# Kernel optimization log

Measured on AMD Instinct MI355X. Metric: run time of the kernel, lower is better.

## Reference

```python
import jax, jax.numpy as jnp
import numpy as np
from functools import partial

NUM_STEPS = 30  # Euler integration steps (inte_steps)


def _point_sample(vol, pts):
    """Trilinear sample of vol [C,D,H,W] at pts [N,3] (voxel coords, (d,h,w) order).
    Matches torch grid_sample(mode='bilinear', padding_mode='border', align_corners=True)
    after the normalize+flip done in PointPooling. Returns [C,N]."""
    dims = jnp.asarray(vol.shape[1:], dtype=pts.dtype)  # (D,H,W)
    p = jnp.clip(pts, 0.0, dims - 1.0)  # border padding == clamp coords
    p0 = jnp.floor(p)
    frac = p - p0  # [N,3]
    i0 = p0.astype(jnp.int32)
    i1 = jnp.minimum(i0 + 1, (dims - 1.0).astype(jnp.int32))
    d0, h0, w0 = i0[:, 0], i0[:, 1], i0[:, 2]
    d1, h1, w1 = i1[:, 0], i1[:, 1], i1[:, 2]
    fd, fh, fw = frac[:, 0], frac[:, 1], frac[:, 2]
    g = lambda d, h, w: vol[:, d, h, w]  # [C,N] gather
    c000, c001 = g(d0, h0, w0), g(d0, h0, w1)
    c010, c011 = g(d0, h1, w0), g(d0, h1, w1)
    c100, c101 = g(d1, h0, w0), g(d1, h0, w1)
    c110, c111 = g(d1, h1, w0), g(d1, h1, w1)
    c00 = c000 * (1 - fw) + c001 * fw
    c01 = c010 * (1 - fw) + c011 * fw
    c10 = c100 * (1 - fw) + c101 * fw
    c11 = c110 * (1 - fw) + c111 * fw
    c0 = c00 * (1 - fh) + c01 * fh
    c1 = c10 * (1 - fh) + c11 * fh
    return c0 * (1 - fd) + c1 * fd  # [C,N]


def _interp(flow, x):
    # flow [B,3,D,H,W], x [B,N,3] -> [B,N,3]
    out = jax.vmap(_point_sample)(flow, x)  # [B,3,N]
    return jnp.transpose(out, (0, 2, 1))


def _integrate_euler(flow, x, num_steps):
    flow = flow * (1.0 / num_steps)
    def step(x, _):
        return x + _interp(flow, x), None
    x, _ = jax.lax.scan(step, x, None, length=num_steps)
    return x


def _forward(verts, affine, flow_field):
    B, N, _ = verts.shape
    ones = jnp.ones((B, N, 1), dtype=verts.dtype)
    homog = jnp.concatenate([verts, ones], axis=-1)  # [B,N,4]
    pred = jnp.einsum('bij,bnj->bni', affine, homog)[..., :3]
    aux = _integrate_euler(flow_field, pred, NUM_STEPS)
    flow_int = aux - pred  # [B,N,3]
    pred = aux
    flow_int = jnp.transpose(flow_int, (0, 2, 1))[..., None, None]  # [B,3,N,1,1]
    homog2 = jnp.concatenate([pred, ones], axis=-1)
    inv_aff = jnp.linalg.inv(affine)
    pred = jnp.einsum('bij,bnj->bni', inv_aff, homog2)[..., :3]
    return pred, flow_int


def setup_inputs() -> dict:
    key = jax.random.key(0)
    k1, k2, k3 = jax.random.split(key, 3)
    B, N = 2, 140000
    D = H = W = 192
    dims = jnp.asarray([D - 1, H - 1, W - 1], dtype=jnp.float32)
    verts = jax.random.uniform(k1, (B, N, 3), dtype=jnp.float32) * dims
    affine = jnp.eye(4, dtype=jnp.float32)[None] + 0.01 * jax.random.normal(k2, (B, 4, 4), dtype=jnp.float32)
    flow_field = jax.random.normal(k3, (B, 3, D, H, W), dtype=jnp.float32)
    return {"verts": verts, "affine": affine, "flow_field": flow_field}


def reference(verts, affine, flow_field):
    return _forward(verts, affine, flow_field)
```

## Files before the change

### kernel.cpp

```cpp
#include <hip/hip_runtime.h>
#include <hip/hip_fp16.h>

#define NSTEPS 30
#define DIM 192
static constexpr long DHW = (long)DIM * DIM * DIM;
static constexpr int PTS_PER_WAVE = 21;

__global__ void invert4x4_kernel(const float* __restrict__ aff,
                                 float* __restrict__ out, int B) {
    int b = blockIdx.x * blockDim.x + threadIdx.x;
    if (b >= B) return;
    double a[16];
#pragma unroll
    for (int i = 0; i < 16; i++) a[i] = (double)aff[b * 16 + i];
    double s0 = a[0]*a[5]  - a[4]*a[1];
    double s1 = a[0]*a[6]  - a[4]*a[2];
    double s2 = a[0]*a[7]  - a[4]*a[3];
    double s3 = a[1]*a[6]  - a[5]*a[2];
    double s4 = a[1]*a[7]  - a[5]*a[3];
    double s5 = a[2]*a[7]  - a[6]*a[3];
    double c5 = a[10]*a[15] - a[14]*a[11];
    double c4 = a[9]*a[15]  - a[13]*a[11];
    double c3 = a[9]*a[14]  - a[13]*a[10];
    double c2 = a[8]*a[15]  - a[12]*a[11];
    double c1 = a[8]*a[14]  - a[12]*a[10];
    double c0 = a[8]*a[13]  - a[12]*a[9];
    double det = s0*c5 - s1*c4 + s2*c3 + s3*c2 - s4*c1 + s5*c0;
    double inv = 1.0 / det;
    double o[16];
    o[0]  = ( a[5]*c5 - a[6]*c4 + a[7]*c3) * inv;
    o[1]  = (-a[1]*c5 + a[2]*c4 - a[3]*c3) * inv;
    o[2]  = ( a[13]*s5 - a[14]*s4 + a[15]*s3) * inv;
    o[3]  = (-a[9]*s5 + a[10]*s4 - a[11]*s3) * inv;
    o[4]  = (-a[4]*c5 + a[6]*c2 - a[7]*c1) * inv;
    o[5]  = ( a[0]*c5 - a[2]*c2 + a[3]*c1) * inv;
    o[6]  = (-a[12]*s5 + a[14]*s2 - a[15]*s1) * inv;
    o[7]  = ( a[8]*s5 - a[10]*s2 + a[11]*s1) * inv;
    o[8]  = ( a[4]*c4 - a[5]*c2 + a[7]*c0) * inv;
    o[9]  = (-a[0]*c4 + a[1]*c2 - a[3]*c0) * inv;
    o[10] = ( a[12]*s4 - a[13]*s2 + a[15]*s0) * inv;
    o[11] = (-a[8]*s4 + a[9]*s2 - a[11]*s0) * inv;
    o[12] = (-a[4]*c3 + a[5]*c1 - a[6]*c0) * inv;
    o[13] = ( a[0]*c3 - a[1]*c1 + a[2]*c0) * inv;
    o[14] = (-a[12]*s3 + a[13]*s1 - a[14]*s0) * inv;
    o[15] = ( a[8]*s3 - a[9]*s1 + a[10]*s0) * inv;
#pragma unroll
    for (int i = 0; i < 16; i++) out[b * 16 + i] = (float)o[i];
}

__global__ __launch_bounds__(256) void repack_kernel(const float* __restrict__ flow,
                                                     __half* __restrict__ packed) {
    long vox = (long)blockIdx.x * blockDim.x + threadIdx.x;
    int b = blockIdx.y;
    if (vox >= DHW) return;
    const float* F = flow + (size_t)b * 3 * DHW;
    float f0 = F[vox];
    float f1 = F[vox + DHW];
    float f2 = F[vox + 2 * DHW];
    union { __half2 h2[2]; int2 i2; } u;
    u.h2[0] = __floats2half2_rn(f0, f1);
    u.h2[1] = __floats2half2_rn(f2, 0.0f);
    reinterpret_cast<int2*>(packed)[(size_t)b * DHW + vox] = u.i2;
}

__global__ __launch_bounds__(256) void deform_packed_kernel(
    const float* __restrict__ verts,
    const float* __restrict__ affine,
    const __half* __restrict__ packed,
    const float* __restrict__ invaff,
    float* __restrict__ out_pred,
    float* __restrict__ out_flow,
    int N, int B) {
    int lane = threadIdx.x & 63;
    int wib  = threadIdx.x >> 6;
    long gwave = (long)blockIdx.x * (blockDim.x >> 6) + wib;

    int piw = lane / 3;
    if (piw > PTS_PER_WAVE - 1) piw = PTS_PER_WAVE - 1;
    int ch = lane - piw * 3;
    if (ch > 2) ch = 2;

    long pt = gwave * PTS_PER_WAVE + piw;
    bool valid = (lane < 63) && (pt < (long)B * N);
    long ptc = valid ? pt : ((long)B * N - 1);
    int b = (int)(ptc / N);
    int n = (int)(ptc - (long)b * N);

    const float* A = affine + b * 16;
    const float* v = verts + (size_t)ptc * 3;
    float vx = v[0], vy = v[1], vz = v[2];
    float x = A[0] * vx + A[1] * vy + A[2]  * vz + A[3];
    float y = A[4] * vx + A[5] * vy + A[6]  * vz + A[7];
    float z = A[8] * vx + A[9] * vy + A[10] * vz + A[11];
    float p0 = (ch == 0) ? x : (ch == 1) ? y : z;

    const __half* Pb = packed + ((size_t)b * DHW) * 4 + ch;
    const float scale = (float)(1.0 / NSTEPS);

    float cc[8];
    int key = -1;
    int bl = piw * 3;

    for (int s = 0; s < NSTEPS; s++) {
        float pd = fminf(fmaxf(x, 0.0f), (float)(DIM - 1));
        float ph = fminf(fmaxf(y, 0.0f), (float)(DIM - 1));
        float pw = fminf(fmaxf(z, 0.0f), (float)(DIM - 1));
        float fd0 = floorf(pd), fh0 = floorf(ph), fw0 = floorf(pw);
        int d0 = (int)fd0, h0 = (int)fh0, w0 = (int)fw0;
        float fd = pd - fd0, fh = ph - fh0, fw = pw - fw0;

        int k = (d0 * DIM + h0) * DIM + w0;
        if (k != key) {
            key = k;
            int d1 = min(d0 + 1, DIM - 1);
            int h1 = min(h0 + 1, DIM - 1);
            int w1 = min(w0 + 1, DIM - 1);
            size_t r00 = (size_t)((d0 * DIM + h0) * DIM) * 4;
            size_t r01 = (size_t)((d0 * DIM + h1) * DIM) * 4;
            size_t r10 = (size_t)((d1 * DIM + h0) * DIM) * 4;
            size_t r11 = (size_t)((d1 * DIM + h1) * DIM) * 4;
            size_t o0 = (size_t)w0 * 4, o1 = (size_t)w1 * 4;
            cc[0] = __half2float(Pb[r00 + o0]) * scale;
            cc[1] = __half2float(Pb[r00 + o1]) * scale;
            cc[2] = __half2float(Pb[r01 + o0]) * scale;
            cc[3] = __half2float(Pb[r01 + o1]) * scale;
            cc[4] = __half2float(Pb[r10 + o0]) * scale;
            cc[5] = __half2float(Pb[r10 + o1]) * scale;
            cc[6] = __half2float(Pb[r11 + o0]) * scale;
            cc[7] = __half2float(Pb[r11 + o1]) * scale;
        }

        float omfw = 1.0f - fw, omfh = 1.0f - fh, omfd = 1.0f - fd;
        float c00 = cc[0] * omfw + cc[1] * fw;
        float c01 = cc[2] * omfw + cc[3] * fw;
        float c10 = cc[4] * omfw + cc[5] * fw;
        float c11 = cc[6] * omfw + cc[7] * fw;
        float c0 = c00 * omfh + c01 * fh;
        float c1 = c10 * omfh + c11 * fh;
        float val = c0 * omfd + c1 * fd;

        float v0 = __shfl(val, bl,     64);
        float v1 = __shfl(val, bl + 1, 64);
        float v2 = __shfl(val, bl + 2, 64);
        x += v0; y += v1; z += v2;
    }

    if (valid) {
        float posc = (ch == 0) ? x : (ch == 1) ? y : z;
        float fint = posc - p0;
        const float* Ai = invaff + b * 16 + ch * 4;
        float o = Ai[0] * x + Ai[1] * y + Ai[2] * z + Ai[3];
        out_pred[(size_t)ptc * 3 + ch] = o;
        out_flow[(size_t)b * 3 * N + (size_t)ch * N + n] = fint;
    }
}

__global__ __launch_bounds__(256) void deform_kernel(
    const float* __restrict__ verts,
    const float* __restrict__ affine,
    const float* __restrict__ flow,
    const float* __restrict__ invaff,
    float* __restrict__ out_pred,
    float* __restrict__ out_flow,
    int N, int B) {
    int lane = threadIdx.x & 63;
    int wib  = threadIdx.x >> 6;
    long gwave = (long)blockIdx.x * (blockDim.x >> 6) + wib;
    int piw = lane / 3;
    if (piw > PTS_PER_WAVE - 1) piw = PTS_PER_WAVE - 1;
    int ch = lane - piw * 3;
    if (ch > 2) ch = 2;
    long pt = gwave * PTS_PER_WAVE + piw;
    bool valid = (lane < 63) && (pt < (long)B * N);
    long ptc = valid ? pt : ((long)B * N - 1);
    int b = (int)(ptc / N);
    int n = (int)(ptc - (long)b * N);
    const float* A = affine + b * 16;
    const float* v = verts + (size_t)ptc * 3;
    float vx = v[0], vy = v[1], vz = v[2];
    float x = A[0] * vx + A[1] * vy + A[2]  * vz + A[3];
    float y = A[4] * vx + A[5] * vy + A[6]  * vz + A[7];
    float z = A[8] * vx + A[9] * vy + A[10] * vz + A[11];
    float p0 = (ch == 0) ? x : (ch == 1) ? y : z;
    const float* Fc = flow + ((size_t)b * 3 + ch) * (size_t)DHW;
    const float scale = (float)(1.0 / NSTEPS);
    float cc[8];
    int key = -1;
    int bl = piw * 3;
    for (int s = 0; s < NSTEPS; s++) {
        float pd = fminf(fmaxf(x, 0.0f), (float)(DIM - 1));
        float ph = fminf(fmaxf(y, 0.0f), (float)(DIM - 1));
        float pw = fminf(fmaxf(z, 0.0f), (float)(DIM - 1));
        float fd0 = floorf(pd), fh0 = floorf(ph), fw0 = floorf(pw);
        int d0 = (int)fd0, h0 = (int)fh0, w0 = (int)fw0;
        float fd = pd - fd0, fh = ph - fh0, fw = pw - fw0;
        int k = (d0 * DIM + h0) * DIM + w0;
        if (k != key) {
            key = k;
            int d1 = min(d0 + 1, DIM - 1);
            int h1 = min(h0 + 1, DIM - 1);
            int w1 = min(w0 + 1, DIM - 1);
            int r00 = (d0 * DIM + h0) * DIM;
            int r01 = (d0 * DIM + h1) * DIM;
            int r10 = (d1 * DIM + h0) * DIM;
            int r11 = (d1 * DIM + h1) * DIM;
            cc[0] = Fc[r00 + w0] * scale;
            cc[1] = Fc[r00 + w1] * scale;
            cc[2] = Fc[r01 + w0] * scale;
            cc[3] = Fc[r01 + w1] * scale;
            cc[4] = Fc[r10 + w0] * scale;
            cc[5] = Fc[r10 + w1] * scale;
            cc[6] = Fc[r11 + w0] * scale;
            cc[7] = Fc[r11 + w1] * scale;
        }
        float omfw = 1.0f - fw, omfh = 1.0f - fh, omfd = 1.0f - fd;
        float c00 = cc[0] * omfw + cc[1] * fw;
        float c01 = cc[2] * omfw + cc[3] * fw;
        float c10 = cc[4] * omfw + cc[5] * fw;
        float c11 = cc[6] * omfw + cc[7] * fw;
        float c0 = c00 * omfh + c01 * fh;
        float c1 = c10 * omfh + c11 * fh;
        float val = c0 * omfd + c1 * fd;
        float v0 = __shfl(val, bl,     64);
        float v1 = __shfl(val, bl + 1, 64);
        float v2 = __shfl(val, bl + 2, 64);
        x += v0; y += v1; z += v2;
    }
    if (valid) {
        float posc = (ch == 0) ? x : (ch == 1) ? y : z;
        float fint = posc - p0;
        const float* Ai = invaff + b * 16 + ch * 4;
        float o = Ai[0] * x + Ai[1] * y + Ai[2] * z + Ai[3];
        out_pred[(size_t)ptc * 3 + ch] = o;
        out_flow[(size_t)b * 3 * N + (size_t)ch * N + n] = fint;
    }
}

extern "C" void kernel_launch(void* const* d_in, const int* in_sizes, int n_in,
                              void* d_out, int out_size, void* d_ws, size_t ws_size,
                              hipStream_t stream) {
    const float* verts  = (const float*)d_in[0];
    const float* affine = (const float*)d_in[1];
    const float* flow   = (const float*)d_in[2];

    int B = in_sizes[1] / 16;
    int N = in_sizes[0] / (3 * B);

    float* out_pred = (float*)d_out;
    float* out_flow = out_pred + (size_t)B * N * 3;

    size_t packed_bytes = (size_t)B * DHW * 4 * sizeof(__half);
    bool use_packed = (ws_size >= packed_bytes + 256);

    long total_pts = (long)B * N;
    long waves  = (total_pts + PTS_PER_WAVE - 1) / PTS_PER_WAVE;
    long blocks = (waves + 3) / 4;

    if (use_packed) {
        __half* packed = (__half*)d_ws;
        float* invaff  = (float*)((char*)d_ws + packed_bytes);
        hipLaunchKernelGGL(invert4x4_kernel, dim3(1), dim3(64), 0, stream,
                           affine, invaff, B);
        long vblocks = (DHW + 255) / 256;
        hipLaunchKernelGGL(repack_kernel, dim3((unsigned)vblocks, B), dim3(256), 0,
                           stream, flow, packed);
        hipLaunchKernelGGL(deform_packed_kernel, dim3((unsigned)blocks), dim3(256),
                           0, stream, verts, affine, packed, invaff,
                           out_pred, out_flow, N, B);
    } else {
        float* invaff = (float*)d_ws;
        hipLaunchKernelGGL(invert4x4_kernel, dim3(1), dim3(64), 0, stream,
                           affine, invaff, B);
        hipLaunchKernelGGL(deform_kernel, dim3((unsigned)blocks), dim3(256), 0,
                           stream, verts, affine, flow, invaff,
                           out_pred, out_flow, N, B);
    }
}
```

Baseline: 306.1 us.

## Sort points into spatial bins and vectorize flow repack for gather locality

Adds a counting sort of points by their initial voxel coordinates into 16^3-voxel bins (histogram with atomics, single-block scan, atomic scatter into a permutation). The deform kernel then processes points in permuted order, and blocks are remapped so each of 8 interleaved groups covers a contiguous range. The aim is better L2/cache locality for the trilinear gathers over the packed half-precision flow volume. The repack kernel is also vectorized to handle four voxels per thread with float4 loads and int4 stores. This adds several small kernel launches and a memset, and the scatter order is nondeterministic.

```diff
diff --git a/kernel.cpp b/kernel.cpp
--- a/kernel.cpp
+++ b/kernel.cpp
@@ -5,6 +5,7 @@
 #define DIM 192
 static constexpr long DHW = (long)DIM * DIM * DIM;
 static constexpr int PTS_PER_WAVE = 21;
+static constexpr int NBINS = 12 * 12 * 12;
 
 __global__ void invert4x4_kernel(const float* __restrict__ aff,
                                  float* __restrict__ out, int B) {
@@ -48,41 +49,119 @@
     for (int i = 0; i < 16; i++) out[b * 16 + i] = (float)o[i];
 }
 
-__global__ __launch_bounds__(256) void repack_kernel(const float* __restrict__ flow,
-                                                     __half* __restrict__ packed) {
-    long vox = (long)blockIdx.x * blockDim.x + threadIdx.x;
+__global__ __launch_bounds__(256) void repack4_kernel(const float* __restrict__ flow,
+                                                      __half* __restrict__ packed) {
+    long q = (long)blockIdx.x * blockDim.x + threadIdx.x;
     int b = blockIdx.y;
-    if (vox >= DHW) return;
+    long v0 = q * 4;
+    if (v0 >= DHW) return;
     const float* F = flow + (size_t)b * 3 * DHW;
-    float f0 = F[vox];
-    float f1 = F[vox + DHW];
-    float f2 = F[vox + 2 * DHW];
-    union { __half2 h2[2]; int2 i2; } u;
-    u.h2[0] = __floats2half2_rn(f0, f1);
-    u.h2[1] = __floats2half2_rn(f2, 0.0f);
-    reinterpret_cast<int2*>(packed)[(size_t)b * DHW + vox] = u.i2;
-}
-
-__global__ __launch_bounds__(256) void deform_packed_kernel(
+    float4 f0 = *reinterpret_cast<const float4*>(F + v0);
+    float4 f1 = *reinterpret_cast<const float4*>(F + v0 + DHW);
+    float4 f2 = *reinterpret_cast<const float4*>(F + v0 + 2 * DHW);
+    union { __half2 h[2]; int2 i2; } u;
+    int4 o0, o1;
+    u.h[0] = __floats2half2_rn(f0.x, f1.x); u.h[1] = __floats2half2_rn(f2.x, 0.f);
+    o0.x = u.i2.x; o0.y = u.i2.y;
+    u.h[0] = __floats2half2_rn(f0.y, f1.y); u.h[1] = __floats2half2_rn(f2.y, 0.f);
+    o0.z = u.i2.x; o0.w = u.i2.y;
+    u.h[0] = __floats2half2_rn(f0.z, f1.z); u.h[1] = __floats2half2_rn(f2.z, 0.f);
+    o1.x = u.i2.x; o1.y = u.i2.y;
+    u.h[0] = __floats2half2_rn(f0.w, f1.w); u.h[1] = __floats2half2_rn(f2.w, 0.f);
+    o1.z = u.i2.x; o1.w = u.i2.y;
+    int4* out = reinterpret_cast<int4*>(packed) + (((size_t)b * DHW + v0) >> 1);
+    out[0] = o0;
+    out[1] = o1;
+}
+
+__global__ __launch_bounds__(256) void bin_count_kernel(
+    const float* __restrict__ verts, const float* __restrict__ affine,
+    unsigned* __restrict__ hist, unsigned short* __restrict__ keys, int N, int B) {
+    int i = blockIdx.x * blockDim.x + threadIdx.x;
+    if (i >= B * N) return;
+    int b = i / N;
+    const float* A = affine + b * 16;
+    const float* v = verts + (size_t)i * 3;
+    float vx = v[0], vy = v[1], vz = v[2];
+    float x = A[0] * vx + A[1] * vy + A[2]  * vz + A[3];
+    float y = A[4] * vx + A[5] * vy + A[6]  * vz + A[7];
+    float z = A[8] * vx + A[9] * vy + A[10] * vz + A[11];
+    int d0 = (int)floorf(fminf(fmaxf(x, 0.0f), (float)(DIM - 1)));
+    int h0 = (int)floorf(fminf(fmaxf(y, 0.0f), (float)(DIM - 1)));
+    int w0 = (int)floorf(fminf(fmaxf(z, 0.0f), (float)(DIM - 1)));
+    unsigned key = ((unsigned)(d0 >> 4) * 12 + (unsigned)(h0 >> 4)) * 12
+                 + (unsigned)(w0 >> 4);
+    keys[i] = (unsigned short)key;
+    atomicAdd(&hist[key], 1u);
+}
+
+__global__ __launch_bounds__(256) void scan_bins_kernel(
+    const unsigned* __restrict__ hist, unsigned* __restrict__ offs) {
+    __shared__ unsigned lsum[256];
+    int t = threadIdx.x;
+    unsigned loc[7];
+    unsigned s = 0;
+#pragma unroll
+    for (int j = 0; j < 7; j++) {
+        int i = t * 7 + j;
+        unsigned v = (i < NBINS) ? hist[i] : 0u;
+        loc[j] = s;
+        s += v;
+    }
+    lsum[t] = s;
+    __syncthreads();
+    for (int off = 1; off < 256; off <<= 1) {
+        unsigned v = (t >= off) ? lsum[t - off] : 0u;
+        __syncthreads();
+        lsum[t] += v;
+        __syncthreads();
+    }
+    unsigned base = (t > 0) ? lsum[t - 1] : 0u;
+#pragma unroll
+    for (int j = 0; j < 7; j++) {
+        int i = t * 7 + j;
+        if (i < NBINS) offs[i] = base + loc[j];
+    }
+}
+
+__global__ __launch_bounds__(256) void scatter_kernel(
+    const unsigned short* __restrict__ keys, unsigned* __restrict__ offs,
+    unsigned* __restrict__ perm, int total) {
+    int i = blockIdx.x * blockDim.x + threadIdx.x;
+    if (i >= total) return;
+    unsigned pos = atomicAdd(&offs[keys[i]], 1u);
+    perm[pos] = (unsigned)i;
+}
+
+static __device__ __forceinline__ float2 h2f(unsigned u) {
+    return __half22float2(__builtin_bit_cast(__half2, u));
+}
+
+__global__ __launch_bounds__(256) void deform_sorted_kernel(
     const float* __restrict__ verts,
     const float* __restrict__ affine,
     const __half* __restrict__ packed,
     const float* __restrict__ invaff,
+    const unsigned* __restrict__ perm,
     float* __restrict__ out_pred,
     float* __restrict__ out_flow,
-    int N, int B) {
+    int N, int B, int nblk8) {
+    int bi = blockIdx.x;
+    int lblk = (bi & 7) * (nblk8 >> 3) + (bi >> 3);
     int lane = threadIdx.x & 63;
     int wib  = threadIdx.x >> 6;
-    long gwave = (long)blockIdx.x * (blockDim.x >> 6) + wib;
+    long gwave = (long)lblk * 4 + wib;
 
     int piw = lane / 3;
     if (piw > PTS_PER_WAVE - 1) piw = PTS_PER_WAVE - 1;
     int ch = lane - piw * 3;
     if (ch > 2) ch = 2;
 
-    long pt = gwave * PTS_PER_WAVE + piw;
-    bool valid = (lane < 63) && (pt < (long)B * N);
-    long ptc = valid ? pt : ((long)B * N - 1);
+    long slot = gwave * PTS_PER_WAVE + piw;
+    long total = (long)B * N;
+    bool valid = (lane < 63) && (slot < total);
+    long sc = valid ? slot : total - 1;
+    long ptc = (long)perm[sc];
     int b = (int)(ptc / N);
     int n = (int)(ptc - (long)b * N);
 
@@ -245,32 +324,56 @@
 
     int B = in_sizes[1] / 16;
     int N = in_sizes[0] / (3 * B);
+    long total = (long)B * N;
 
     float* out_pred = (float*)d_out;
     float* out_flow = out_pred + (size_t)B * N * 3;
 
     size_t packed_bytes = (size_t)B * DHW * 4 * sizeof(__half);
-    bool use_packed = (ws_size >= packed_bytes + 256);
-
-    long total_pts = (long)B * N;
-    long waves  = (total_pts + PTS_PER_WAVE - 1) / PTS_PER_WAVE;
-    long blocks = (waves + 3) / 4;
+    size_t off_invaff = packed_bytes;
+    size_t off_hist   = off_invaff + (size_t)B * 16 * sizeof(float);
+    size_t off_offs   = off_hist + NBINS * sizeof(unsigned);
+    size_t off_perm   = off_offs + NBINS * sizeof(unsigned);
+    size_t off_keys   = off_perm + (size_t)total * sizeof(unsigned);
+    size_t need = off_keys + (size_t)total * sizeof(unsigned short) + 256;
+    bool use_packed = (ws_size >= need);
 
     if (use_packed) {
-        __half* packed = (__half*)d_ws;
-        float* invaff  = (float*)((char*)d_ws + packed_bytes);
+        char* ws = (char*)d_ws;
+        __half* packed        = (__half*)ws;
+        float* invaff         = (float*)(ws + off_invaff);
+        unsigned* hist        = (unsigned*)(ws + off_hist);
+        unsigned* offs        = (unsigned*)(ws + off_offs);
+        unsigned* perm        = (unsigned*)(ws + off_perm);
+        unsigned short* keys  = (unsigned short*)(ws + off_keys);
+
         hipLaunchKernelGGL(invert4x4_kernel, dim3(1), dim3(64), 0, stream,
                            affine, invaff, B);
-        long vblocks = (DHW + 255) / 256;
-        hipLaunchKernelGGL(repack_kernel, dim3((unsigned)vblocks, B), dim3(256), 0,
+        long quads = (DHW + 3) / 4;
+        long vblocks = (quads + 255) / 256;
+        hipLaunchKernelGGL(repack4_kernel, dim3((unsigned)vblocks, B), dim3(256), 0,
                            stream, flow, packed);
-        hipLaunchKernelGGL(deform_packed_kernel, dim3((unsigned)blocks), dim3(256),
-                           0, stream, verts, affine, packed, invaff,
-                           out_pred, out_flow, N, B);
+        hipMemsetAsync(hist, 0, NBINS * sizeof(unsigned), stream);
+        int pblocks = (int)((total + 255) / 256);
+        hipLaunchKernelGGL(bin_count_kernel, dim3(pblocks), dim3(256), 0, stream,
+                           verts, affine, hist, keys, N, B);
+        hipLaunchKernelGGL(scan_bins_kernel, dim3(1), dim3(256), 0, stream,
+                           hist, offs);
+        hipLaunchKernelGGL(scatter_kernel, dim3(pblocks), dim3(256), 0, stream,
+                           keys, offs, perm, (int)total);
+
+        long waves  = (total + PTS_PER_WAVE - 1) / PTS_PER_WAVE;
+        long blocks = (waves + 3) / 4;
+        long blocks8 = ((blocks + 7) / 8) * 8;
+        hipLaunchKernelGGL(deform_sorted_kernel, dim3((unsigned)blocks8), dim3(256),
+                           0, stream, verts, affine, packed, invaff, perm,
+                           out_pred, out_flow, N, B, (int)blocks8);
     } else {
         float* invaff = (float*)d_ws;
         hipLaunchKernelGGL(invert4x4_kernel, dim3(1), dim3(64), 0, stream,
                            affine, invaff, B);
+        long waves  = (total + PTS_PER_WAVE - 1) / PTS_PER_WAVE;
+        long blocks = (waves + 3) / 4;
         hipLaunchKernelGGL(deform_kernel, dim3((unsigned)blocks), dim3(256), 0,
                            stream, verts, affine, flow, invaff,
                            out_pred, out_flow, N, B);
```

Result: slower. 418.3 us (+36.7%).
